# Optimization experiments

Measured on AMD Instinct MI355X. Metric: run time of the kernel, lower is better.

Reference implementation:

```python
import jax, jax.numpy as jnp
import numpy as np

FEATURE_DIM = 512
HIDDEN_DIM = 512
N_HEADS = 8
HEAD_DIM = HIDDEN_DIM // N_HEADS
MAX_LEN = 5000
GAMMA = 0.5  # gaussian relative-position bias width
LN_EPS = 1e-5


def make_pe(d_model, max_len):
    # sinusoidal positional encoding buffer, as in PositionalEncoding.__init__
    pos = jnp.arange(max_len, dtype=jnp.float32)[:, None]
    div = jnp.exp(jnp.arange(0, d_model, 2, dtype=jnp.float32) * (-np.log(10000.0) / d_model))
    ang = pos * div  # [max_len, d_model/2]
    pe = jnp.zeros((max_len, d_model), dtype=jnp.float32)
    pe = pe.at[:, 0::2].set(jnp.sin(ang)).at[:, 1::2].set(jnp.cos(ang))
    return pe


def setup_inputs() -> dict:
    key = jax.random.key(0)
    k_x, k_q, k_k, k_v = jax.random.split(key, 4)
    xavier = np.sqrt(6.0 / (FEATURE_DIM + HEAD_DIM))  # xavier_uniform over last two dims
    return {
        "data_window": jax.random.normal(k_x, (1, 2048, FEATURE_DIM), dtype=jnp.float32),
        "W_query": jax.random.uniform(k_q, (N_HEADS, FEATURE_DIM, HEAD_DIM), jnp.float32, -xavier, xavier),
        "W_key": jax.random.uniform(k_k, (N_HEADS, FEATURE_DIM, HEAD_DIM), jnp.float32, -xavier, xavier),
        "W_value": jax.random.uniform(k_v, (N_HEADS, FEATURE_DIM, HEAD_DIM), jnp.float32, -xavier, xavier),
        "ln_gamma": jnp.ones((FEATURE_DIM,), dtype=jnp.float32),
        "ln_beta": jnp.zeros((FEATURE_DIM,), dtype=jnp.float32),
    }


def reference(data_window, W_query, W_key, W_value, ln_gamma, ln_beta):
    B, S, F = data_window.shape
    temperature = 1.0

    # LayerNorm over feature dim
    mu = jnp.mean(data_window, axis=-1, keepdims=True)
    var = jnp.mean(jnp.square(data_window - mu), axis=-1, keepdims=True)
    x = (data_window - mu) * jax.lax.rsqrt(var + LN_EPS) * ln_gamma + ln_beta

    # positional encoding, exactly as original: x + pe[:x.shape[0]] (requires B==1)
    pe = make_pe(FEATURE_DIM, MAX_LEN)
    x = x + pe[:B]  # [B,F] broadcasts over [B,S,F] only because B==1

    # per-head QKV projections, vectorized over heads
    Q = jnp.einsum('bsf,hfd->bhsd', x, W_query)
    K = jnp.einsum('bsf,hfd->bhsd', x, W_key)
    V = jnp.einsum('bsf,hfd->bhsd', x, W_value)

    scores = jnp.einsum('bhsd,bhtd->bhst', Q, K) / np.sqrt(HEAD_DIM)

    # gaussian relative-position bias: scale(=1) * exp(-gamma * (i-j)^2)
    p = jnp.arange(S, dtype=jnp.float32)
    rel = p[:, None] - p[None, :]
    bias = jnp.exp(-GAMMA * jnp.square(rel))  # [S,S]
    scores = (scores + bias[None, None]) / temperature
    # dropout on scores is identity in eval mode

    attn = jax.nn.softmax(scores, axis=-1)  # [B,H,S,S]
    head_out = jnp.einsum('bhst,bhtd->bhsd', attn, V)

    # concat heads along feature dim: [B,S,H*D]
    multi_head_output = head_out.transpose(0, 2, 1, 3).reshape(B, S, N_HEADS * HEAD_DIM)
    mean_weights = jnp.mean(attn, axis=1)  # [B,S,S]
    return multi_head_output, mean_weights
```

## Files before the change

### kernel.cpp

```cpp
#include <hip/hip_runtime.h>
#include <hip/hip_bf16.h>
#include <math.h>

#define S_LEN 2048
#define FDIM  512
#define NH    8
#define HD    64
#define MH_ELEMS (S_LEN * FDIM)
#define MEAN_ELEMS (S_LEN * S_LEN)
#define LOG2E 1.44269504f
#define QK_SCALE_L2 0.18033688f
#define SM_SHIFT 10.0f

typedef _Float16 half_t;
typedef _Float16 half2v __attribute__((ext_vector_type(2)));
typedef _Float16 half4v __attribute__((ext_vector_type(4)));
typedef _Float16 half8v __attribute__((ext_vector_type(8)));
typedef float    float4v __attribute__((ext_vector_type(4)));
typedef int      int4v   __attribute__((ext_vector_type(4)));

#define MFMA16(a, b, c) __builtin_amdgcn_mfma_f32_16x16x32_f16((a), (b), (c), 0, 0, 0)

static __device__ __forceinline__ float fast_exp2(float x) {
    return __builtin_amdgcn_exp2f(x);
}

__global__ __launch_bounds__(256) void prep_kernel(const float* __restrict__ x,
                                                   const float* __restrict__ gamma,
                                                   const float* __restrict__ beta,
                                                   const float* __restrict__ Wq,
                                                   const float* __restrict__ Wk,
                                                   const float* __restrict__ Wv,
                                                   half_t* __restrict__ xo,
                                                   half_t* __restrict__ WT) {
    const int tid = threadIdx.x;
    if (blockIdx.x < 2048) {
        const int row = blockIdx.x;
        const float2 v = ((const float2*)(x + (size_t)row * FDIM))[tid];
        float s = v.x + v.y;
        float q = v.x * v.x + v.y * v.y;
        #pragma unroll
        for (int off = 1; off < 64; off <<= 1) {
            s += __shfl_xor(s, off, 64);
            q += __shfl_xor(q, off, 64);
        }
        __shared__ float red[8];
        const int wave = tid >> 6;
        if ((tid & 63) == 0) { red[wave] = s; red[4 + wave] = q; }
        __syncthreads();
        s = red[0] + red[1] + red[2] + red[3];
        q = red[4] + red[5] + red[6] + red[7];
        const float mu  = s * (1.0f / FDIM);
        const float var = q * (1.0f / FDIM) - mu * mu;
        const float rstd = rsqrtf(var + 1e-5f);
        const int f0 = tid * 2, f1 = tid * 2 + 1;
        const float o0 = (v.x - mu) * rstd * gamma[f0] + beta[f0];
        const float o1 = (v.y - mu) * rstd * gamma[f1] + beta[f1] + 1.0f;
        half2v o; o.x = (half_t)o0; o.y = (half_t)o1;
        ((half2v*)(xo + (size_t)row * FDIM))[tid] = o;
    } else {
        const int idx = blockIdx.x - 2048;
        const int k0 = (idx & 7) * 64;
        const int h  = (idx >> 3) & 7;
        const int z  = idx >> 6;
        const float* W = ((z == 0) ? Wq : (z == 1) ? Wk : Wv) + (size_t)h * FDIM * HD;
        __shared__ float Ls[64][65];
        {
            const int kk = tid >> 2, dg = (tid & 3) * 16;
            #pragma unroll
            for (int j = 0; j < 4; ++j) {
                const float4 w = *(const float4*)(W + (size_t)(k0 + kk) * HD + dg + j * 4);
                Ls[kk][dg + j * 4 + 0] = w.x; Ls[kk][dg + j * 4 + 1] = w.y;
                Ls[kk][dg + j * 4 + 2] = w.z; Ls[kk][dg + j * 4 + 3] = w.w;
            }
        }
        __syncthreads();
        {
            const int d = tid >> 2, kg = (tid & 3) * 16;
            half8v t0, t1;
            #pragma unroll
            for (int j = 0; j < 8; ++j) t0[j] = (half_t)Ls[kg + j][d];
            #pragma unroll
            for (int j = 0; j < 8; ++j) t1[j] = (half_t)Ls[kg + 8 + j][d];
            half_t* dst = WT + ((size_t)(z * NH + h) * HD + d) * FDIM + k0 + kg;
            *(half8v*)dst = t0;
            *(half8v*)(dst + 8) = t1;
        }
    }
}

__global__ __launch_bounds__(256) void qkv_kernel(const half_t* __restrict__ xh,
                                                  const half_t* __restrict__ WT,
                                                  half_t* __restrict__ Qo,
                                                  half_t* __restrict__ Ko,
                                                  half_t* __restrict__ VTo) {
    const int ms0 = blockIdx.x * 128;
    const int h   = blockIdx.y, z = blockIdx.z;
    const half_t* Wt = WT + (size_t)(z * NH + h) * HD * FDIM;

    const int tid = threadIdx.x;
    const int wv = tid >> 6, lane = tid & 63;
    const int lo = lane & 15, qq = lane >> 4;

    float4v acc[2][4];
    #pragma unroll
    for (int rg = 0; rg < 2; ++rg)
        #pragma unroll
        for (int cg = 0; cg < 4; ++cg) acc[rg][cg] = (float4v){0.f, 0.f, 0.f, 0.f};

    const half_t* ar[2];
    ar[0] = xh + (size_t)(ms0 + wv * 32 + lo) * FDIM + qq * 8;
    ar[1] = ar[0] + 16 * FDIM;
    const half_t* wrow[4];
    #pragma unroll
    for (int cg = 0; cg < 4; ++cg) wrow[cg] = Wt + (size_t)(cg * 16 + lo) * FDIM + qq * 8;

    half8v a_c[2][2], b_c[4][2];
    #pragma unroll
    for (int rg = 0; rg < 2; ++rg) { a_c[rg][0] = *(const half8v*)(ar[rg]); a_c[rg][1] = *(const half8v*)(ar[rg] + 32); }
    #pragma unroll
    for (int cg = 0; cg < 4; ++cg) { b_c[cg][0] = *(const half8v*)(wrow[cg]); b_c[cg][1] = *(const half8v*)(wrow[cg] + 32); }

    for (int k0 = 0; k0 < FDIM; k0 += 64) {
        const int kn0 = (k0 + 64 < FDIM) ? k0 + 64 : 0;
        const int kn1 = (k0 + 96 < FDIM) ? k0 + 96 : 0;
        half8v a_n[2][2], b_n[4][2];
        #pragma unroll
        for (int rg = 0; rg < 2; ++rg) { a_n[rg][0] = *(const half8v*)(ar[rg] + kn0); a_n[rg][1] = *(const half8v*)(ar[rg] + kn1); }
        #pragma unroll
        for (int cg = 0; cg < 4; ++cg) { b_n[cg][0] = *(const half8v*)(wrow[cg] + kn0); b_n[cg][1] = *(const half8v*)(wrow[cg] + kn1); }
        #pragma unroll
        for (int kh = 0; kh < 2; ++kh)
            #pragma unroll
            for (int rg = 0; rg < 2; ++rg)
                #pragma unroll
                for (int cg = 0; cg < 4; ++cg)
                    acc[rg][cg] = MFMA16(a_c[rg][kh], b_c[cg][kh], acc[rg][cg]);
        #pragma unroll
        for (int rg = 0; rg < 2; ++rg) { a_c[rg][0] = a_n[rg][0]; a_c[rg][1] = a_n[rg][1]; }
        #pragma unroll
        for (int cg = 0; cg < 4; ++cg) { b_c[cg][0] = b_n[cg][0]; b_c[cg][1] = b_n[cg][1]; }
    }

    if (z < 2) {
        half_t* Co = ((z == 0) ? Qo : Ko) + (size_t)h * S_LEN * HD;
        #pragma unroll
        for (int rg = 0; rg < 2; ++rg)
            #pragma unroll
            for (int cg = 0; cg < 4; ++cg)
                #pragma unroll
                for (int r = 0; r < 4; ++r)
                    Co[(size_t)(ms0 + wv * 32 + rg * 16 + qq * 4 + r) * HD + cg * 16 + lo] =
                        (half_t)acc[rg][cg][r];
    } else {
        __shared__ float Ls[128][65];
        #pragma unroll
        for (int rg = 0; rg < 2; ++rg)
            #pragma unroll
            for (int cg = 0; cg < 4; ++cg)
                #pragma unroll
                for (int r = 0; r < 4; ++r)
                    Ls[wv * 32 + rg * 16 + qq * 4 + r][cg * 16 + lo] = acc[rg][cg][r];
        __syncthreads();
        const int d = tid & 63, sg = tid >> 6;
        half_t* dst = VTo + (size_t)(h * HD + d) * S_LEN + ms0 + sg * 32;
        #pragma unroll
        for (int c = 0; c < 4; ++c) {
            half8v t;
            #pragma unroll
            for (int j = 0; j < 8; ++j) t[j] = (half_t)Ls[sg * 32 + c * 8 + j][d];
            *(half8v*)(dst + c * 8) = t;
        }
    }
}

__global__ __launch_bounds__(256) void attn2_kernel(const half_t* __restrict__ Qw,
                                                    const half_t* __restrict__ Kw,
                                                    const half_t* __restrict__ VT,
                                                    half_t* __restrict__ Op,
                                                    float* __restrict__ lp) {
    const int s0 = blockIdx.x * 32;
    const int h  = blockIdx.y;
    const int z  = blockIdx.z;
    const half_t* Qh = Qw + (size_t)h * S_LEN * HD;
    const half_t* Kh = Kw + (size_t)h * S_LEN * HD;
    const half_t* Vt = VT + (size_t)h * (size_t)HD * S_LEN;

    __shared__ float Osh[4][32][65];
    __shared__ float lsh[4][32];

    const int tid = threadIdx.x;
    const int wv = tid >> 6, lane = tid & 63;
    const int lo = lane & 15, qq = lane >> 4;
    const int tb = z * 1024 + wv * 256;

    const half8v qA0 = *(const half8v*)(Qh + (size_t)(s0 + lo) * HD + qq * 8);
    const half8v qA1 = *(const half8v*)(Qh + (size_t)(s0 + lo) * HD + 32 + qq * 8);
    const half8v qB0 = *(const half8v*)(Qh + (size_t)(s0 + 16 + lo) * HD + qq * 8);
    const half8v qB1 = *(const half8v*)(Qh + (size_t)(s0 + 16 + lo) * HD + 32 + qq * 8);

    float4v accA[4], accB[4];
    #pragma unroll
    for (int dt = 0; dt < 4; ++dt) {
        accA[dt] = (float4v){0.f, 0.f, 0.f, 0.f};
        accB[dt] = (float4v){0.f, 0.f, 0.f, 0.f};
    }
    float lA = 0.f, lB = 0.f;

    const int srcLow  = lo + ((qq & 1) * 2) * 16;
    const int srcHigh = srcLow + 16;
    const bool sel1 = (qq >> 1) != 0;

    half8v kc[4];
    {
        const half_t* kp0 = Kh + (size_t)(tb + lo) * HD;
        const half_t* kp1 = Kh + (size_t)(tb + 16 + lo) * HD;
        kc[0] = *(const half8v*)(kp0 + qq * 8);
        kc[1] = *(const half8v*)(kp0 + 32 + qq * 8);
        kc[2] = *(const half8v*)(kp1 + qq * 8);
        kc[3] = *(const half8v*)(kp1 + 32 + qq * 8);
    }

    for (int ps = 0; ps < 8; ++ps) {
        const int Tg  = tb + ps * 32;
        const int Tgn = tb + ((ps < 7) ? ps + 1 : ps) * 32;
        half8v kn[4], vc[4];
        {
            const half_t* kp0 = Kh + (size_t)(Tgn + lo) * HD;
            const half_t* kp1 = Kh + (size_t)(Tgn + 16 + lo) * HD;
            kn[0] = *(const half8v*)(kp0 + qq * 8);
            kn[1] = *(const half8v*)(kp0 + 32 + qq * 8);
            kn[2] = *(const half8v*)(kp1 + qq * 8);
            kn[3] = *(const half8v*)(kp1 + 32 + qq * 8);
            #pragma unroll
            for (int dt = 0; dt < 4; ++dt)
                vc[dt] = *(const half8v*)(Vt + (size_t)(dt * 16 + lo) * S_LEN + Tg + qq * 8);
        }
        float4v c0A = (float4v){0.f, 0.f, 0.f, 0.f};
        c0A = MFMA16(kc[0], qA0, c0A); c0A = MFMA16(kc[1], qA1, c0A);
        float4v c1A = (float4v){0.f, 0.f, 0.f, 0.f};
        c1A = MFMA16(kc[2], qA0, c1A); c1A = MFMA16(kc[3], qA1, c1A);
        float4v c0B = (float4v){0.f, 0.f, 0.f, 0.f};
        c0B = MFMA16(kc[0], qB0, c0B); c0B = MFMA16(kc[1], qB1, c0B);
        float4v c1B = (float4v){0.f, 0.f, 0.f, 0.f};
        c1B = MFMA16(kc[2], qB0, c1B); c1B = MFMA16(kc[3], qB1, c1B);

        const int dd0 = s0 - Tg;
        const bool nA0 = (dd0 > -40) && (dd0 < 40);
        const bool nA1 = (dd0 - 16 > -40) && (dd0 - 16 < 40);
        const bool nB0 = (dd0 + 16 > -40) && (dd0 + 16 < 40);
        const bool nB1 = nA0;
        float E0A[4], E1A[4], E0B[4], E1B[4];
        float lsA = 0.f, lsB = 0.f;
        #pragma unroll
        for (int r = 0; r < 4; ++r) {
            const int t0 = Tg + qq * 4 + r, t1 = t0 + 16;
            float sa0 = c0A[r] * QK_SCALE_L2 - SM_SHIFT;
            if (nA0) { const float d = (float)(s0 + lo - t0); sa0 += __expf(-0.5f * d * d) * LOG2E; }
            float sa1 = c1A[r] * QK_SCALE_L2 - SM_SHIFT;
            if (nA1) { const float d = (float)(s0 + lo - t1); sa1 += __expf(-0.5f * d * d) * LOG2E; }
            float sb0 = c0B[r] * QK_SCALE_L2 - SM_SHIFT;
            if (nB0) { const float d = (float)(s0 + 16 + lo - t0); sb0 += __expf(-0.5f * d * d) * LOG2E; }
            float sb1 = c1B[r] * QK_SCALE_L2 - SM_SHIFT;
            if (nB1) { const float d = (float)(s0 + 16 + lo - t1); sb1 += __expf(-0.5f * d * d) * LOG2E; }
            E0A[r] = fast_exp2(sa0); E1A[r] = fast_exp2(sa1);
            E0B[r] = fast_exp2(sb0); E1B[r] = fast_exp2(sb1);
            lsA += E0A[r] + E1A[r];
            lsB += E0B[r] + E1B[r];
        }
        lA += lsA;
        lB += lsB;

        int pkA0, pkA1, pkA2, pkA3, pkB0, pkB1, pkB2, pkB3;
        {
            half2v p;
            p.x = (half_t)E0A[0]; p.y = (half_t)E0A[1]; pkA0 = __builtin_bit_cast(int, p);
            p.x = (half_t)E0A[2]; p.y = (half_t)E0A[3]; pkA1 = __builtin_bit_cast(int, p);
            p.x = (half_t)E1A[0]; p.y = (half_t)E1A[1]; pkA2 = __builtin_bit_cast(int, p);
            p.x = (half_t)E1A[2]; p.y = (half_t)E1A[3]; pkA3 = __builtin_bit_cast(int, p);
            p.x = (half_t)E0B[0]; p.y = (half_t)E0B[1]; pkB0 = __builtin_bit_cast(int, p);
            p.x = (half_t)E0B[2]; p.y = (half_t)E0B[3]; pkB1 = __builtin_bit_cast(int, p);
            p.x = (half_t)E1B[0]; p.y = (half_t)E1B[1]; pkB2 = __builtin_bit_cast(int, p);
            p.x = (half_t)E1B[2]; p.y = (half_t)E1B[3]; pkB3 = __builtin_bit_cast(int, p);
        }
        int4v biA, biB;
        {
            const int l0a = __shfl(pkA0, srcLow, 64),  l0b = __shfl(pkA2, srcLow, 64);
            const int l1a = __shfl(pkA1, srcLow, 64),  l1b = __shfl(pkA3, srcLow, 64);
            const int h0a = __shfl(pkA0, srcHigh, 64), h0b = __shfl(pkA2, srcHigh, 64);
            const int h1a = __shfl(pkA1, srcHigh, 64), h1b = __shfl(pkA3, srcHigh, 64);
            biA[0] = sel1 ? l0b : l0a;
            biA[1] = sel1 ? l1b : l1a;
            biA[2] = sel1 ? h0b : h0a;
            biA[3] = sel1 ? h1b : h1a;
        }
        {
            const int l0a = __shfl(pkB0, srcLow, 64),  l0b = __shfl(pkB2, srcLow, 64);
            const int l1a = __shfl(pkB1, srcLow, 64),  l1b = __shfl(pkB3, srcLow, 64);
            const int h0a = __shfl(pkB0, srcHigh, 64), h0b = __shfl(pkB2, srcHigh, 64);
            const int h1a = __shfl(pkB1, srcHigh, 64), h1b = __shfl(pkB3, srcHigh, 64);
            biB[0] = sel1 ? l0b : l0a;
            biB[1] = sel1 ? l1b : l1a;
            biB[2] = sel1 ? h0b : h0a;
            biB[3] = sel1 ? h1b : h1a;
        }
        const half8v bpA = __builtin_bit_cast(half8v, biA);
        const half8v bpB = __builtin_bit_cast(half8v, biB);
        #pragma unroll
        for (int dt = 0; dt < 4; ++dt) {
            accA[dt] = MFMA16(vc[dt], bpA, accA[dt]);
            accB[dt] = MFMA16(vc[dt], bpB, accB[dt]);
        }
        #pragma unroll
        for (int i = 0; i < 4; ++i) kc[i] = kn[i];
    }

    lA += __shfl_xor(lA, 16, 64); lA += __shfl_xor(lA, 32, 64);
    lB += __shfl_xor(lB, 16, 64); lB += __shfl_xor(lB, 32, 64);
    if (qq == 0) {
        lsh[wv][lo] = lA;
        lsh[wv][16 + lo] = lB;
    }
    #pragma unroll
    for (int dt = 0; dt < 4; ++dt)
        #pragma unroll
        for (int r = 0; r < 4; ++r) {
            Osh[wv][lo][dt * 16 + qq * 4 + r]      = accA[dt][r];
            Osh[wv][16 + lo][dt * 16 + qq * 4 + r] = accB[dt][r];
        }
    __syncthreads();

    #pragma unroll
    for (int p = 0; p < 2; ++p) {
        const int q = p * 16 + (tid >> 4), dg = tid & 15;
        const float L = lsh[0][q] + lsh[1][q] + lsh[2][q] + lsh[3][q];
        const float inv = 1.0f / L;
        half4v o;
        #pragma unroll
        for (int i = 0; i < 4; ++i) {
            const float ov = Osh[0][q][dg * 4 + i] + Osh[1][q][dg * 4 + i] +
                             Osh[2][q][dg * 4 + i] + Osh[3][q][dg * 4 + i];
            o[i] = (half_t)(ov * inv);
        }
        const size_t pidx = (size_t)(z * NH + h) * S_LEN + s0 + q;
        *(half4v*)(Op + pidx * HD + dg * 4) = o;
        if (dg == 0) lp[pidx] = L;
    }
}

__global__ __launch_bounds__(256) void mean2_kernel(const half_t* __restrict__ Qw,
                                                    const half_t* __restrict__ Kw,
                                                    const half_t* __restrict__ Op,
                                                    const float* __restrict__ lp,
                                                    float* __restrict__ out) {
    const int q0 = blockIdx.x * 32;
    const int tbase = blockIdx.y * 256;
    const int tid = threadIdx.x;

    __shared__ float lnc[NH][32];
    __shared__ float g0s[NH][32];
    __shared__ float g1s[NH][32];
    {
        const int h = tid >> 5, qi = tid & 31;
        const size_t i0 = (size_t)h * S_LEN + q0 + qi;
        const size_t i1 = (size_t)(NH + h) * S_LEN + q0 + qi;
        const float l0 = lp[i0], l1 = lp[i1];
        const float L = l0 + l1;
        const float inv = 1.0f / L;
        lnc[h][qi] = -__logf(L) * LOG2E - SM_SHIFT;
        g0s[h][qi] = l0 * inv;
        g1s[h][qi] = l1 * inv;
    }
    __syncthreads();

    const int wv = tid >> 6, lane = tid & 63;
    const int lo = lane & 15, qq = lane >> 4;
    const int t0 = tbase + wv * 64;

    float4v macc[2][4];
    #pragma unroll
    for (int rg = 0; rg < 2; ++rg)
        #pragma unroll
        for (int tg = 0; tg < 4; ++tg) macc[rg][tg] = (float4v){0.f, 0.f, 0.f, 0.f};

    const half_t* qp = Qw + (size_t)(q0 + lo) * HD + qq * 8;
    const half_t* kp = Kw + (size_t)(t0 + lo) * HD + qq * 8;

    #pragma unroll 2
    for (int h = 0; h < NH; ++h) {
        half8v a[2][2], b[4][2];
        #pragma unroll
        for (int rg = 0; rg < 2; ++rg) {
            a[rg][0] = *(const half8v*)(qp + (size_t)rg * 16 * HD);
            a[rg][1] = *(const half8v*)(qp + (size_t)rg * 16 * HD + 32);
        }
        #pragma unroll
        for (int tg = 0; tg < 4; ++tg) {
            b[tg][0] = *(const half8v*)(kp + (size_t)tg * 16 * HD);
            b[tg][1] = *(const half8v*)(kp + (size_t)tg * 16 * HD + 32);
        }
        float4v sacc[2][4];
        #pragma unroll
        for (int rg = 0; rg < 2; ++rg)
            #pragma unroll
            for (int tg = 0; tg < 4; ++tg) sacc[rg][tg] = (float4v){0.f, 0.f, 0.f, 0.f};
        #pragma unroll
        for (int kh = 0; kh < 2; ++kh)
            #pragma unroll
            for (int rg = 0; rg < 2; ++rg)
                #pragma unroll
                for (int tg = 0; tg < 4; ++tg)
                    sacc[rg][tg] = MFMA16(a[rg][kh], b[tg][kh], sacc[rg][tg]);

        const float4v ln0 = *(const float4v*)&lnc[h][qq * 4];
        const float4v ln1 = *(const float4v*)&lnc[h][16 + qq * 4];
        #pragma unroll
        for (int tg = 0; tg < 4; ++tg)
            #pragma unroll
            for (int r = 0; r < 4; ++r) {
                macc[0][tg][r] += fast_exp2(fmaf(sacc[0][tg][r], QK_SCALE_L2, ln0[r]));
                macc[1][tg][r] += fast_exp2(fmaf(sacc[1][tg][r], QK_SCALE_L2, ln1[r]));
            }
        qp += (size_t)S_LEN * HD;
        kp += (size_t)S_LEN * HD;
    }

    #pragma unroll
    for (int rg = 0; rg < 2; ++rg)
        #pragma unroll
        for (int tg = 0; tg < 4; ++tg) {
            const int tgl = t0 + tg * 16;
            const bool near = ((q0 + 31 - tgl) > -40) && ((q0 - (tgl + 15)) < 40);
            #pragma unroll
            for (int r = 0; r < 4; ++r) {
                const int qe = q0 + rg * 16 + qq * 4 + r;
                const int te = tgl + lo;
                float w = macc[rg][tg][r] * 0.125f;
                if (near) {
                    const float d = (float)(qe - te);
                    w *= __expf(__expf(-0.5f * d * d));
                }
                out[MH_ELEMS + (size_t)qe * S_LEN + te] = w;
            }
        }

    if (blockIdx.y == 0) {
        const int qi = tid >> 3, dg = (tid & 7) * 8;
        const int q = q0 + qi;
        #pragma unroll
        for (int h = 0; h < NH; ++h) {
            const half8v o0 = *(const half8v*)(Op + ((size_t)h * S_LEN + q) * HD + dg);
            const half8v o1 = *(const half8v*)(Op + ((size_t)(NH + h) * S_LEN + q) * HD + dg);
            const float a0 = g0s[h][qi], a1 = g1s[h][qi];
            float4 r0, r1;
            r0.x = (float)o0[0] * a0 + (float)o1[0] * a1;
            r0.y = (float)o0[1] * a0 + (float)o1[1] * a1;
            r0.z = (float)o0[2] * a0 + (float)o1[2] * a1;
            r0.w = (float)o0[3] * a0 + (float)o1[3] * a1;
            r1.x = (float)o0[4] * a0 + (float)o1[4] * a1;
            r1.y = (float)o0[5] * a0 + (float)o1[5] * a1;
            r1.z = (float)o0[6] * a0 + (float)o1[6] * a1;
            r1.w = (float)o0[7] * a0 + (float)o1[7] * a1;
            float* dst = out + (size_t)q * FDIM + h * HD + dg;
            *(float4*)dst = r0;
            *(float4*)(dst + 4) = r1;
        }
    }
}

extern "C" void kernel_launch(void* const* d_in, const int* in_sizes, int n_in,
                              void* d_out, int out_size, void* d_ws, size_t ws_size,
                              hipStream_t stream) {
    const float* x  = (const float*)d_in[0];
    const float* Wq = (const float*)d_in[1];
    const float* Wk = (const float*)d_in[2];
    const float* Wv = (const float*)d_in[3];
    const float* g  = (const float*)d_in[4];
    const float* b  = (const float*)d_in[5];
    float* out = (float*)d_out;
    char*  ws  = (char*)d_ws;

    half_t* Qh   = (half_t*)(ws);
    half_t* Kh   = (half_t*)(ws + (2ull  << 20));
    half_t* VT   = (half_t*)(ws + (4ull  << 20));
    half_t* xh   = (half_t*)(ws + (6ull  << 20));
    half_t* WT   = (half_t*)(ws + (8ull  << 20));
    half_t* Op   = (half_t*)(ws + (10ull << 20));
    float*  lp   = (float*) (ws + (14ull << 20));

    prep_kernel<<<2240, 256, 0, stream>>>(x, g, b, Wq, Wk, Wv, xh, WT);
    qkv_kernel<<<dim3(16, 8, 3), 256, 0, stream>>>(xh, WT, Qh, Kh, VT);
    attn2_kernel<<<dim3(64, 8, 2), 256, 0, stream>>>(Qh, Kh, VT, Op, lp);
    mean2_kernel<<<dim3(64, 8), 256, 0, stream>>>(Qh, Kh, Op, lp, out);
}
```

Measured before the change: 158.8 us.

## Merge key-split attention into 8-wave blocks writing final output directly

The attention kernel no longer splits keys across two z-blocks of 4 waves. It now runs 512-thread blocks whose 8 waves cover all 2048 keys and reduce in shared memory. The block writes the normalized fp32 head output straight to the output buffer, so the fp16 partial buffer and the combine step in the mean kernel go away. This costs more shared memory per block (about 66KB) and halves the block count to 512, which may reduce occupancy and latency hiding.

```diff
diff --git a/kernel.cpp b/kernel.cpp
--- a/kernel.cpp
+++ b/kernel.cpp
@@ -174,25 +174,24 @@
     }
 }
 
-__global__ __launch_bounds__(256) void attn2_kernel(const half_t* __restrict__ Qw,
+__global__ __launch_bounds__(512) void attn2_kernel(const half_t* __restrict__ Qw,
                                                     const half_t* __restrict__ Kw,
                                                     const half_t* __restrict__ VT,
-                                                    half_t* __restrict__ Op,
+                                                    float* __restrict__ out,
                                                     float* __restrict__ lp) {
     const int s0 = blockIdx.x * 32;
     const int h  = blockIdx.y;
-    const int z  = blockIdx.z;
     const half_t* Qh = Qw + (size_t)h * S_LEN * HD;
     const half_t* Kh = Kw + (size_t)h * S_LEN * HD;
     const half_t* Vt = VT + (size_t)h * (size_t)HD * S_LEN;
 
-    __shared__ float Osh[4][32][65];
-    __shared__ float lsh[4][32];
+    __shared__ float Osh[8][32][65];
+    __shared__ float lsh[8][32];
 
     const int tid = threadIdx.x;
     const int wv = tid >> 6, lane = tid & 63;
     const int lo = lane & 15, qq = lane >> 4;
-    const int tb = z * 1024 + wv * 256;
+    const int tb = wv * 256;
 
     const half8v qA0 = *(const half8v*)(Qh + (size_t)(s0 + lo) * HD + qq * 8);
     const half8v qA1 = *(const half8v*)(Qh + (size_t)(s0 + lo) * HD + 32 + qq * 8);
@@ -330,27 +329,29 @@
         }
     __syncthreads();
 
-    #pragma unroll
-    for (int p = 0; p < 2; ++p) {
-        const int q = p * 16 + (tid >> 4), dg = tid & 15;
-        const float L = lsh[0][q] + lsh[1][q] + lsh[2][q] + lsh[3][q];
+    {
+        const int q = tid >> 4, dg = tid & 15;
+        float L = 0.f;
+        #pragma unroll
+        for (int w = 0; w < 8; ++w) L += lsh[w][q];
         const float inv = 1.0f / L;
-        half4v o;
+        float4 o;
+        float sv[4];
         #pragma unroll
         for (int i = 0; i < 4; ++i) {
-            const float ov = Osh[0][q][dg * 4 + i] + Osh[1][q][dg * 4 + i] +
-                             Osh[2][q][dg * 4 + i] + Osh[3][q][dg * 4 + i];
-            o[i] = (half_t)(ov * inv);
-        }
-        const size_t pidx = (size_t)(z * NH + h) * S_LEN + s0 + q;
-        *(half4v*)(Op + pidx * HD + dg * 4) = o;
-        if (dg == 0) lp[pidx] = L;
+            float s = 0.f;
+            #pragma unroll
+            for (int w = 0; w < 8; ++w) s += Osh[w][q][dg * 4 + i];
+            sv[i] = s * inv;
+        }
+        o.x = sv[0]; o.y = sv[1]; o.z = sv[2]; o.w = sv[3];
+        *(float4*)(out + (size_t)(s0 + q) * FDIM + h * HD + dg * 4) = o;
+        if (dg == 0) lp[(size_t)h * S_LEN + s0 + q] = L;
     }
 }
 
 __global__ __launch_bounds__(256) void mean2_kernel(const half_t* __restrict__ Qw,
                                                     const half_t* __restrict__ Kw,
-                                                    const half_t* __restrict__ Op,
                                                     const float* __restrict__ lp,
                                                     float* __restrict__ out) {
     const int q0 = blockIdx.x * 32;
@@ -358,18 +359,10 @@
     const int tid = threadIdx.x;
 
     __shared__ float lnc[NH][32];
-    __shared__ float g0s[NH][32];
-    __shared__ float g1s[NH][32];
     {
         const int h = tid >> 5, qi = tid & 31;
-        const size_t i0 = (size_t)h * S_LEN + q0 + qi;
-        const size_t i1 = (size_t)(NH + h) * S_LEN + q0 + qi;
-        const float l0 = lp[i0], l1 = lp[i1];
-        const float L = l0 + l1;
-        const float inv = 1.0f / L;
+        const float L = lp[(size_t)h * S_LEN + q0 + qi];
         lnc[h][qi] = -__logf(L) * LOG2E - SM_SHIFT;
-        g0s[h][qi] = l0 * inv;
-        g1s[h][qi] = l1 * inv;
     }
     __syncthreads();
 
@@ -443,29 +436,6 @@
                 out[MH_ELEMS + (size_t)qe * S_LEN + te] = w;
             }
         }
-
-    if (blockIdx.y == 0) {
-        const int qi = tid >> 3, dg = (tid & 7) * 8;
-        const int q = q0 + qi;
-        #pragma unroll
-        for (int h = 0; h < NH; ++h) {
-            const half8v o0 = *(const half8v*)(Op + ((size_t)h * S_LEN + q) * HD + dg);
-            const half8v o1 = *(const half8v*)(Op + ((size_t)(NH + h) * S_LEN + q) * HD + dg);
-            const float a0 = g0s[h][qi], a1 = g1s[h][qi];
-            float4 r0, r1;
-            r0.x = (float)o0[0] * a0 + (float)o1[0] * a1;
-            r0.y = (float)o0[1] * a0 + (float)o1[1] * a1;
-            r0.z = (float)o0[2] * a0 + (float)o1[2] * a1;
-            r0.w = (float)o0[3] * a0 + (float)o1[3] * a1;
-            r1.x = (float)o0[4] * a0 + (float)o1[4] * a1;
-            r1.y = (float)o0[5] * a0 + (float)o1[5] * a1;
-            r1.z = (float)o0[6] * a0 + (float)o1[6] * a1;
-            r1.w = (float)o0[7] * a0 + (float)o1[7] * a1;
-            float* dst = out + (size_t)q * FDIM + h * HD + dg;
-            *(float4*)dst = r0;
-            *(float4*)(dst + 4) = r1;
-        }
-    }
 }
 
 extern "C" void kernel_launch(void* const* d_in, const int* in_sizes, int n_in,
@@ -485,11 +455,10 @@
     half_t* VT   = (half_t*)(ws + (4ull  << 20));
     half_t* xh   = (half_t*)(ws + (6ull  << 20));
     half_t* WT   = (half_t*)(ws + (8ull  << 20));
-    half_t* Op   = (half_t*)(ws + (10ull << 20));
-    float*  lp   = (float*) (ws + (14ull << 20));
+    float*  lp   = (float*) (ws + (10ull << 20));
 
     prep_kernel<<<2240, 256, 0, stream>>>(x, g, b, Wq, Wk, Wv, xh, WT);
     qkv_kernel<<<dim3(16, 8, 3), 256, 0, stream>>>(xh, WT, Qh, Kh, VT);
-    attn2_kernel<<<dim3(64, 8, 2), 256, 0, stream>>>(Qh, Kh, VT, Op, lp);
-    mean2_kernel<<<dim3(64, 8), 256, 0, stream>>>(Qh, Kh, Op, lp, out);
-}
+    attn2_kernel<<<dim3(64, 8), 512, 0, stream>>>(Qh, Kh, VT, out, lp);
+    mean2_kernel<<<dim3(64, 8), 256, 0, stream>>>(Qh, Kh, lp, out);
+}
```

After: 158.7 us. No clear change (-0.1%).
